# Performance work log

Hardware: AMD Instinct MI355X
Metric: run time of the kernel (lower is better)

## Reference

```python
import jax, jax.numpy as jnp
import numpy as np

N_IN = 1024
N_OUT = 1024
L, B = 2048, 16


def setup_inputs() -> dict:
    key = jax.random.key(0)
    k1, k2 = jax.random.split(key, 2)
    val = (3.0 / N_IN) ** 0.5  # matches init_weight uniform range
    return {
        "x": jax.random.normal(k1, (L, B, N_IN), dtype=jnp.float32),
        "c0": jnp.zeros((B, N_OUT), dtype=jnp.float32),
        "weight": jax.random.uniform(k2, (N_IN, 3 * N_OUT), dtype=jnp.float32, minval=-val, maxval=val),
        "bias": jnp.zeros((2 * N_OUT,), dtype=jnp.float32),
    }


def reference(x, c0, weight, bias):
    # x: (L, B, n_in); weight: (n_in, 3*n_out); bias: (2*n_out,)
    Lx, Bx, _ = x.shape
    # u_ = x @ W, viewed as (L, B, n_out, k=3); bidir=1 dropped
    u = (x.reshape(Lx * Bx, N_IN) @ weight).reshape(Lx, Bx, N_OUT, 3)
    x_tilde = u[..., 0]                                  # (L, B, d)
    forget = jax.nn.sigmoid(u[..., 1] + bias[:N_OUT])    # (L, B, d)
    # sequential SRU recurrence: c_t = (c_{t-1} - x~_t) * f_t + x~_t
    def step(c_prev, inputs):
        xt, ft = inputs
        c = (c_prev - xt) * ft + xt
        return c, c
    c_final, cs = jax.lax.scan(step, c0, (x_tilde, forget))
    h = jnp.tanh(cs)  # activation_type == 1 (tanh); no highway, no dropout (eval)
    return h, c_final
```

## Files before the change

kernel.cpp:

```cpp
#include <hip/hip_runtime.h>


typedef __attribute__((ext_vector_type(8))) short short8;
typedef __attribute__((ext_vector_type(4))) float f32x4;

#define L_SEQ 2048
#define BATCH 16
#define NIN   1024
#define NOUT  1024
#define MROWS (L_SEQ * BATCH)
#define NCOLS (2 * NOUT)
#define ROWELEMS (BATCH * NOUT)
#define NCHUNK 32
#define CHLEN  64
#define NT 16

__device__ __forceinline__ unsigned short f2bf(float f) {
  unsigned u = __float_as_uint(f);
  u += 0x7fffu + ((u >> 16) & 1u);
  return (unsigned short)(u >> 16);
}
__device__ __forceinline__ float bf2f(unsigned short b) {
  return __uint_as_float(((unsigned)b) << 16);
}
__device__ __forceinline__ float sigmoidf_(float x) {
  return __builtin_amdgcn_rcpf(1.f + __expf(-x));
}
__device__ __forceinline__ float fast_tanh(float x) {
  float ax = fabsf(x);
  float t = __expf(-2.f * ax);
  float r = (1.f - t) * __builtin_amdgcn_rcpf(1.f + t);
  return copysignf(r, x);
}

#define GLL16(gptr, lptr)                                              \
  __builtin_amdgcn_global_load_lds(                                    \
      (const __attribute__((address_space(1))) void*)(gptr),           \
      (__attribute__((address_space(3))) void*)(lptr), 16, 0, 0)

__global__ __launch_bounds__(256) void cvt_x_k(const float* __restrict__ x,
                                               unsigned short* __restrict__ o) {
  size_t i = ((size_t)blockIdx.x * 256 + threadIdx.x) * 8;
  const float4* p = (const float4*)(x + i);
  float4 a = p[0], b = p[1];
  union { unsigned short s[8]; uint4 v; } r;
  r.s[0] = f2bf(a.x); r.s[1] = f2bf(a.y); r.s[2] = f2bf(a.z); r.s[3] = f2bf(a.w);
  r.s[4] = f2bf(b.x); r.s[5] = f2bf(b.y); r.s[6] = f2bf(b.z); r.s[7] = f2bf(b.w);
  *(uint4*)(o + i) = r.v;
}

__global__ __launch_bounds__(256) void pack_w_k(const float* __restrict__ W,
                                                unsigned short* __restrict__ Bp) {
  int tid = blockIdx.x * 256 + threadIdx.x;
  int k = tid & (NIN - 1);
  int n = tid >> 10;
  int col = 3 * (n >> 1) + (n & 1);
  Bp[tid] = f2bf(W[(size_t)k * (3 * NOUT) + col]);
}

#define BARR __builtin_amdgcn_s_barrier()
#define SCHED0 __builtin_amdgcn_sched_barrier(0)
#define VMCNT(n) asm volatile("s_waitcnt vmcnt(" #n ")" ::: "memory")

#define STAGE_A(bufc, ha, kt)                                                   \
  do {                                                                          \
    GLL16(pga##ha##0 + (kt) * 64, lds + (bufc) * 32768 + (ha) * 16384 + tid * 16);      \
    GLL16(pga##ha##1 + (kt) * 64, lds + (bufc) * 32768 + (ha) * 16384 + 8192 + tid * 16); \
  } while (0)
#define STAGE_B(bufc, hb, kt)                                                   \
  do {                                                                          \
    GLL16(pgb##hb##0 + (kt) * 64, lds + 65536 + (bufc) * 32768 + (hb) * 16384 + tid * 16); \
    GLL16(pgb##hb##1 + (kt) * 64, lds + 65536 + (bufc) * 32768 + (hb) * 16384 + 8192 + tid * 16); \
  } while (0)

#define LDA(DST, bufc, half)                                                    \
  _Pragma("unroll") for (int i = 0; i < 4; ++i) {                               \
    DST[i][0] = *(const short8*)(lds + (bufc) * 32768 + (half) * 16384 +        \
                                 (rowAb + i * 16) * 128 + colX0);               \
    DST[i][1] = *(const short8*)(lds + (bufc) * 32768 + (half) * 16384 +        \
                                 (rowAb + i * 16) * 128 + colX1);               \
  }
#define LDB(DST, bufc, half)                                                    \
  _Pragma("unroll") for (int j = 0; j < 2; ++j) {                               \
    DST[j][0] = *(const short8*)(lds + 65536 + (bufc) * 32768 + (half) * 16384 + \
                                 (rowBb + j * 16) * 128 + colX0);               \
    DST[j][1] = *(const short8*)(lds + 65536 + (bufc) * 32768 + (half) * 16384 + \
                                 (rowBb + j * 16) * 128 + colX1);               \
  }

#define MM(Q, AF, BF)                                                           \
  _Pragma("unroll") for (int i = 0; i < 4; ++i)                                 \
  _Pragma("unroll") for (int j = 0; j < 2; ++j) {                               \
    Q[i][j] = __builtin_amdgcn_mfma_f32_16x16x32_bf16(AF[i][0], BF[j][0], Q[i][j], 0, 0, 0); \
    Q[i][j] = __builtin_amdgcn_mfma_f32_16x16x32_bf16(AF[i][1], BF[j][1], Q[i][j], 0, 0, 0); \
  }

#define PH_TAIL(Q, AF, BF)                                                      \
  BARR;                                                                         \
  __builtin_amdgcn_s_setprio(1);                                                \
  MM(Q, AF, BF);                                                                \
  __builtin_amdgcn_s_setprio(0);                                                \
  BARR;                                                                         \
  SCHED0

#define PH_TAILV(Q, AF, BF)                                                     \
  BARR;                                                                         \
  __builtin_amdgcn_s_setprio(1);                                                \
  MM(Q, AF, BF);                                                                \
  __builtin_amdgcn_s_setprio(0);                                                \
  VMCNT(4);                                                                     \
  BARR;                                                                         \
  SCHED0

#define EPI(Q, qm, qn)                                                          \
  do {                                                                          \
    _Pragma("unroll") for (int i = 0; i < 4; ++i)                               \
    _Pragma("unroll") for (int j = 0; j < 2; ++j) {                             \
      int n = n0 + (qn) * 128 + wn * 32 + j * 16 + nc;                          \
      float bsel = bias[n >> 1];                                                \
      _Pragma("unroll") for (int r = 0; r < 4; ++r) {                           \
        int m = m0 + (qm) * 128 + wm * 64 + i * 16 + mr + r;                    \
        float v = Q[i][j][r];                                                   \
        if (isf) v = sigmoidf_(v + bsel);                                       \
        U[(size_t)m * NCOLS + n] = f2bf(v);                                     \
      }                                                                         \
    }                                                                           \
  } while (0)

__global__ __launch_bounds__(512, 2) void gemm8_k(const unsigned short* __restrict__ A,
                                                  const unsigned short* __restrict__ B,
                                                  const float* __restrict__ bias,
                                                  unsigned short* __restrict__ U) {
  __shared__ __align__(16) char lds[131072];
  const int K = NIN;
  int tid = threadIdx.x;
  int wave = tid >> 6;
  int lane = tid & 63;
  int wm = wave >> 2;
  int wn = wave & 3;
  int lr = lane & 15;
  int hi = lane >> 4;

  int bi = blockIdx.x;
  int t = (bi & 7) * 128 + (bi >> 3);
  int n0 = (t & 7) << 8;
  int m0 = (t >> 3) << 8;

  int rowAb = wm * 64 + lr;
  int rowBb = wn * 32 + lr;
  int swz = (lr & 7) << 4;
  int colX0 = (hi * 16) ^ swz;
  int colX1 = (64 + hi * 16) ^ swz;

  int row0 = tid >> 3;
  int gch = (tid & 7) ^ (row0 & 7);
  const unsigned short* pga00 = A + (size_t)(m0 + row0) * K + gch * 8;
  const unsigned short* pga01 = pga00 + (size_t)64 * K;
  const unsigned short* pga10 = pga00 + (size_t)128 * K;
  const unsigned short* pga11 = pga00 + (size_t)192 * K;
  const unsigned short* pgb00 = B + (size_t)(n0 + row0) * K + gch * 8;
  const unsigned short* pgb01 = pgb00 + (size_t)64 * K;
  const unsigned short* pgb10 = pgb00 + (size_t)128 * K;
  const unsigned short* pgb11 = pgb00 + (size_t)192 * K;

  f32x4 zero = {0.f, 0.f, 0.f, 0.f};
  f32x4 acc00[4][2], acc01[4][2], acc11[4][2], acc10[4][2];
#pragma unroll
  for (int i = 0; i < 4; ++i)
#pragma unroll
    for (int j = 0; j < 2; ++j) {
      acc00[i][j] = zero; acc01[i][j] = zero;
      acc11[i][j] = zero; acc10[i][j] = zero;
    }

  short8 af[4][2], bq0[2][2], bq1[2][2];

  STAGE_A(0, 0, 0); STAGE_A(0, 1, 0); STAGE_B(0, 0, 0); STAGE_B(0, 1, 0);
  STAGE_A(1, 0, 1); STAGE_B(1, 1, 1);
  VMCNT(4);
  BARR;
  SCHED0;

  for (int it = 0; it < NT / 2; ++it) {
    int kt = it * 2;
    int k1 = kt + 1, k2 = (kt + 2) & (NT - 1), k3 = (kt + 3) & (NT - 1);
    STAGE_B(1, 0, k1); STAGE_A(1, 1, k1);
    LDA(af, 0, 0); LDB(bq0, 0, 0);
    PH_TAIL(acc00, af, bq0);
    LDB(bq1, 0, 1);
    PH_TAIL(acc01, af, bq1);
    STAGE_A(0, 0, k2);
    LDA(af, 0, 1);
    PH_TAIL(acc11, af, bq1);
    STAGE_B(0, 1, k2);
    PH_TAILV(acc10, af, bq0);
    STAGE_A(0, 1, k2);
    LDA(af, 1, 0); LDB(bq0, 1, 0);
    PH_TAIL(acc00, af, bq0);
    STAGE_B(0, 0, k2);
    LDB(bq1, 1, 1);
    PH_TAIL(acc01, af, bq1);
    STAGE_A(1, 0, k3);
    LDA(af, 1, 1);
    PH_TAIL(acc11, af, bq1);
    STAGE_B(1, 1, k3);
    PH_TAILV(acc10, af, bq0);
  }
  VMCNT(0);

  int mr = hi * 4;
  int nc = lane & 15;
  bool isf = nc & 1;
  EPI(acc00, 0, 0);
  EPI(acc01, 0, 1);
  EPI(acc11, 1, 1);
  EPI(acc10, 1, 0);
}

__global__ __launch_bounds__(256) void scan_p1(const unsigned int* __restrict__ U2,
                                               float2* __restrict__ AV) {
  int tid = threadIdx.x;
  int bid = blockIdx.x;
  int bd = ((bid >> 7) << 10) + ((bid & 3) << 8) + tid;
  int chunk = (bid >> 2) & 31;
  const unsigned int* up = U2 + (size_t)chunk * CHLEN * ROWELEMS + bd;
  float a = 1.f, v = 0.f;
  for (int t0 = 0; t0 < CHLEN; t0 += 8) {
    unsigned int w[8];
#pragma unroll
    for (int j = 0; j < 8; ++j) w[j] = up[(size_t)(t0 + j) * ROWELEMS];
#pragma unroll
    for (int j = 0; j < 8; ++j) {
      float xt = bf2f((unsigned short)(w[j] & 0xffffu));
      float f  = bf2f((unsigned short)(w[j] >> 16));
      v = f * v + (1.f - f) * xt;
      a = a * f;
    }
  }
  AV[(size_t)chunk * ROWELEMS + bd] = make_float2(a, v);
}

__global__ __launch_bounds__(256) void scan_p2(const float2* __restrict__ AV,
                                               const float* __restrict__ c0,
                                               float* __restrict__ CS,
                                               float* __restrict__ out) {
  int bd = blockIdx.x * 256 + threadIdx.x;
  float c = c0[bd];
  float2 av[NCHUNK];
#pragma unroll
  for (int k = 0; k < NCHUNK; ++k) av[k] = AV[(size_t)k * ROWELEMS + bd];
#pragma unroll
  for (int k = 0; k < NCHUNK; ++k) {
    CS[(size_t)k * ROWELEMS + bd] = c;
    c = av[k].x * c + av[k].y;
  }
  out[(size_t)MROWS * NOUT + bd] = c;
}

__global__ __launch_bounds__(256) void scan_p3(const unsigned int* __restrict__ U2,
                                               const float* __restrict__ CS,
                                               float* __restrict__ out) {
  int tid = threadIdx.x;
  int bid = blockIdx.x;
  int bd = ((bid >> 7) << 10) + ((bid & 3) << 8) + tid;
  int chunk = (bid >> 2) & 31;
  float c = CS[(size_t)chunk * ROWELEMS + bd];
  const unsigned int* up = U2 + (size_t)chunk * CHLEN * ROWELEMS + bd;
  float* op = out + (size_t)chunk * CHLEN * ROWELEMS + bd;
  for (int t0 = 0; t0 < CHLEN; t0 += 8) {
    unsigned int w[8];
#pragma unroll
    for (int j = 0; j < 8; ++j) w[j] = up[(size_t)(t0 + j) * ROWELEMS];
#pragma unroll
    for (int j = 0; j < 8; ++j) {
      float xt = bf2f((unsigned short)(w[j] & 0xffffu));
      float f  = bf2f((unsigned short)(w[j] >> 16));
      c = (c - xt) * f + xt;
      op[(size_t)(t0 + j) * ROWELEMS] = fast_tanh(c);
    }
  }
}

extern "C" void kernel_launch(void* const* d_in, const int* in_sizes, int n_in,
                              void* d_out, int out_size, void* d_ws, size_t ws_size,
                              hipStream_t stream) {
  const float* x    = (const float*)d_in[0];
  const float* c0   = (const float*)d_in[1];
  const float* W    = (const float*)d_in[2];
  const float* bias = (const float*)d_in[3];
  float* out = (float*)d_out;

  char* ws = (char*)d_ws;
  unsigned short* Abf = (unsigned short*)ws;
  unsigned short* Bp  = (unsigned short*)(ws + ((size_t)64 << 20));
  unsigned short* U   = (unsigned short*)(ws + ((size_t)68 << 20));
  float2* AV = (float2*)ws;
  float*  CS = (float*)(ws + ((size_t)4 << 20));

  cvt_x_k<<<MROWS * NIN / (256 * 8), 256, 0, stream>>>(x, Abf);
  pack_w_k<<<NCOLS * NIN / 256, 256, 0, stream>>>(W, Bp);
  gemm8_k<<<1024, 512, 0, stream>>>(Abf, Bp, bias, U);
  scan_p1<<<2048, 256, 0, stream>>>((const unsigned int*)U, AV);
  scan_p2<<<64, 256, 0, stream>>>(AV, c0, CS, out);
  scan_p3<<<2048, 256, 0, stream>>>((const unsigned int*)U, CS, out);
}
```

Before: 257.6 us.

## Fuse chunked scan passes into single-pass decoupled lookback kernel; tile weight pack

Replaces the three-kernel chunked scan (chunk aggregates, carry propagation, apply) with one kernel. Blocks take ordered tickets, publish per-chunk aggregates with flags, and spin-wait on earlier chunks before applying the recurrence from register-held inputs. This avoids rereading U and the extra launches, at the cost of serial lookback over up to 31 predecessors and spin-wait contention. The weight pack kernel is also rewritten to transpose through LDS with 16-byte stores instead of strided scalar reads. The fused path runs only when the workspace is large enough, otherwise the old three kernels are used.

```diff
diff --git a/kernel.cpp b/kernel.cpp
--- a/kernel.cpp
+++ b/kernel.cpp
@@ -13,6 +13,7 @@
 #define ROWELEMS (BATCH * NOUT)
 #define NCHUNK 32
 #define CHLEN  64
+#define NPANEL 64
 #define NT 16
 
 __device__ __forceinline__ unsigned short f2bf(float f) {
@@ -51,11 +52,27 @@
 
 __global__ __launch_bounds__(256) void pack_w_k(const float* __restrict__ W,
                                                 unsigned short* __restrict__ Bp) {
-  int tid = blockIdx.x * 256 + threadIdx.x;
-  int k = tid & (NIN - 1);
-  int n = tid >> 10;
-  int col = 3 * (n >> 1) + (n & 1);
-  Bp[tid] = f2bf(W[(size_t)k * (3 * NOUT) + col]);
+  __shared__ float tile[64][97];
+  int n0 = blockIdx.x * 64;
+  int k0 = blockIdx.y * 64;
+  int c0 = 3 * (n0 >> 1);
+  int tid = threadIdx.x;
+  for (int idx = tid; idx < 64 * 96; idx += 256) {
+    int r = idx / 96, c = idx - r * 96;
+    tile[r][c] = W[(size_t)(k0 + r) * (3 * NOUT) + c0 + c];
+  }
+  __syncthreads();
+#pragma unroll
+  for (int q = 0; q < 2; ++q) {
+    int pos = tid * 2 + q;
+    int dn = pos >> 3;
+    int j8 = (pos & 7) * 8;
+    int cl = 3 * (dn >> 1) + (dn & 1);
+    union { unsigned short s[8]; uint4 v; } r;
+#pragma unroll
+    for (int j = 0; j < 8; ++j) r.s[j] = f2bf(tile[j8 + j][cl]);
+    *(uint4*)(Bp + (size_t)(n0 + dn) * NIN + k0 + j8) = r.v;
+  }
 }
 
 #define BARR __builtin_amdgcn_s_barrier()
@@ -217,6 +234,97 @@
   EPI(acc10, 1, 0);
 }
 
+__global__ __launch_bounds__(256) void clear_k(int* __restrict__ p) {
+  int i = blockIdx.x * 256 + threadIdx.x;
+  if (i < NCHUNK * NPANEL + 1) p[i] = 0;
+}
+
+__global__ __launch_bounds__(256) void scan_fused(const unsigned int* __restrict__ U2,
+                                                  const float* __restrict__ c0,
+                                                  float2* __restrict__ AV,
+                                                  int* __restrict__ flags,
+                                                  int* __restrict__ ticket,
+                                                  float* __restrict__ out) {
+  __shared__ int s_ticket;
+  int tid = threadIdx.x;
+  if (tid == 0) s_ticket = atomicAdd(ticket, 1);
+  __syncthreads();
+  int v = s_ticket;
+  int ci = (v >> 6) & (NCHUNK - 1);
+  int p = v & (NPANEL - 1);
+  int bd = (p << 8) + tid;
+  int lane = tid & 63;
+
+  const unsigned int* up = U2 + (size_t)ci * CHLEN * ROWELEMS + bd;
+  unsigned int u[CHLEN];
+#pragma unroll
+  for (int t = 0; t < CHLEN; ++t) u[t] = up[(size_t)t * ROWELEMS];
+
+  float a = 1.f, vv = 0.f;
+#pragma unroll
+  for (int t = 0; t < CHLEN; ++t) {
+    float xt = bf2f((unsigned short)(u[t] & 0xffffu));
+    float f  = bf2f((unsigned short)(u[t] >> 16));
+    vv = f * vv + (1.f - f) * xt;
+    a = a * f;
+  }
+  {
+    unsigned long long w =
+        ((unsigned long long)__float_as_uint(vv) << 32) | __float_as_uint(a);
+    __hip_atomic_store((unsigned long long*)&AV[(size_t)ci * ROWELEMS + bd], w,
+                       __ATOMIC_RELAXED, __HIP_MEMORY_SCOPE_AGENT);
+  }
+  __threadfence();
+  __syncthreads();
+  if (tid == 0)
+    __hip_atomic_store(&flags[ci * NPANEL + p], 1, __ATOMIC_RELEASE,
+                       __HIP_MEMORY_SCOPE_AGENT);
+
+  float c = c0[bd];
+  if (ci > 0) {
+    int done = (lane < ci) ? 0 : 1;
+    long long spins = 0;
+    bool timeout = false;
+    while (!__all(done)) {
+      if (!done)
+        done = __hip_atomic_load(&flags[lane * NPANEL + p], __ATOMIC_ACQUIRE,
+                                 __HIP_MEMORY_SCOPE_AGENT);
+      if (++spins > (1ll << 24)) { timeout = true; break; }
+    }
+    __threadfence();
+    if (!timeout) {
+      for (int l = 0; l < ci; ++l) {
+        unsigned long long w = __hip_atomic_load(
+            (const unsigned long long*)&AV[(size_t)l * ROWELEMS + bd],
+            __ATOMIC_RELAXED, __HIP_MEMORY_SCOPE_AGENT);
+        float al = __uint_as_float((unsigned)(w & 0xffffffffull));
+        float vl = __uint_as_float((unsigned)(w >> 32));
+        c = al * c + vl;
+      }
+    } else {
+      for (int l = 0; l < ci; ++l) {
+        const unsigned int* vp = U2 + (size_t)l * CHLEN * ROWELEMS + bd;
+        for (int t = 0; t < CHLEN; ++t) {
+          unsigned int w = vp[(size_t)t * ROWELEMS];
+          float xt = bf2f((unsigned short)(w & 0xffffu));
+          float f  = bf2f((unsigned short)(w >> 16));
+          c = (c - xt) * f + xt;
+        }
+      }
+    }
+  }
+
+  float* op = out + (size_t)ci * CHLEN * ROWELEMS + bd;
+#pragma unroll
+  for (int t = 0; t < CHLEN; ++t) {
+    float xt = bf2f((unsigned short)(u[t] & 0xffffu));
+    float f  = bf2f((unsigned short)(u[t] >> 16));
+    c = (c - xt) * f + xt;
+    op[(size_t)t * ROWELEMS] = fast_tanh(c);
+  }
+  if (ci == NCHUNK - 1) out[(size_t)MROWS * NOUT + bd] = c;
+}
+
 __global__ __launch_bounds__(256) void scan_p1(const unsigned int* __restrict__ U2,
                                                float2* __restrict__ AV) {
   int tid = threadIdx.x;
@@ -294,13 +402,26 @@
   unsigned short* Abf = (unsigned short*)ws;
   unsigned short* Bp  = (unsigned short*)(ws + ((size_t)64 << 20));
   unsigned short* U   = (unsigned short*)(ws + ((size_t)68 << 20));
-  float2* AV = (float2*)ws;
-  float*  CS = (float*)(ws + ((size_t)4 << 20));
+
+  const size_t HIGH = (size_t)196 << 20;
+  bool lookback = ws_size >= HIGH + ((size_t)4 << 20) + 16384;
 
   cvt_x_k<<<MROWS * NIN / (256 * 8), 256, 0, stream>>>(x, Abf);
-  pack_w_k<<<NCOLS * NIN / 256, 256, 0, stream>>>(W, Bp);
+  pack_w_k<<<dim3(NCOLS / 64, NIN / 64), 256, 0, stream>>>(W, Bp);
   gemm8_k<<<1024, 512, 0, stream>>>(Abf, Bp, bias, U);
-  scan_p1<<<2048, 256, 0, stream>>>((const unsigned int*)U, AV);
-  scan_p2<<<64, 256, 0, stream>>>(AV, c0, CS, out);
-  scan_p3<<<2048, 256, 0, stream>>>((const unsigned int*)U, CS, out);
-}
+
+  if (lookback) {
+    float2* AV  = (float2*)(ws + HIGH);
+    int* flags  = (int*)(ws + HIGH + ((size_t)4 << 20));
+    int* ticket = flags + NCHUNK * NPANEL;
+    clear_k<<<9, 256, 0, stream>>>(flags);
+    scan_fused<<<NCHUNK * NPANEL, 256, 0, stream>>>((const unsigned int*)U, c0,
+                                                    AV, flags, ticket, out);
+  } else {
+    float2* AV = (float2*)ws;
+    float*  CS = (float*)(ws + ((size_t)4 << 20));
+    scan_p1<<<2048, 256, 0, stream>>>((const unsigned int*)U, AV);
+    scan_p2<<<64, 256, 0, stream>>>(AV, c0, CS, out);
+    scan_p3<<<2048, 256, 0, stream>>>((const unsigned int*)U, CS, out);
+  }
+}
```

After: 790.2 us. 3.07x slower.
